# Performance work log

Hardware: AMD Instinct MI355X
Metric: run time of the kernel (lower is better)

The kernel has to match this reference:

```python
import jax, jax.numpy as jnp
import numpy as np

B, D, H = 32768, 512, 512


def setup_inputs() -> dict:
    key = jax.random.key(0)
    ks = jax.random.split(key, 20)
    stdv = 1.0 / np.sqrt(H)

    def u(k, shape):
        return jax.random.uniform(k, shape, jnp.float32, -stdv, stdv)

    inp = {
        "input": jax.random.normal(ks[0], (B, D), jnp.float32),
        "h": jax.random.normal(ks[1], (B, H), jnp.float32),
        "c": jax.random.normal(ks[2], (B, H), jnp.float32),
    }
    names = ["w_ii", "w_hi", "b_ii", "b_hi", "w_if", "w_hf", "b_if", "b_hf",
             "w_ig", "w_hg", "b_ig", "b_hg", "w_io", "w_ho", "b_io", "b_ho"]
    shapes = {"w_i": (D, H), "w_h": (H, H), "b_": (H,)}
    for i, n in enumerate(names):
        shp = (D, H) if n.startswith("w_i") else ((H, H) if n.startswith("w_h") else (H,))
        inp[n] = u(ks[3 + i], shp)
    return inp


def lstm_cell(input, h, c,
              w_ii, w_hi, b_ii, b_hi, w_if, w_hf, b_if, b_hf,
              w_ig, w_hg, b_ig, b_hg, w_io, w_ho, b_io, b_ho):
    # Fuse the 8 small GEMMs into 2 concatenated GEMMs: [B,D]@[D,4H], [B,H]@[H,4H].
    w_x = jnp.concatenate([w_ii, w_if, w_ig, w_io], axis=1)   # [D, 4H]
    w_h = jnp.concatenate([w_hi, w_hf, w_hg, w_ho], axis=1)   # [H, 4H]
    b = jnp.concatenate([b_ii + b_hi, b_if + b_hf, b_ig + b_hg, b_io + b_ho])  # [4H]
    pre = input @ w_x + h @ w_h + b                            # [B, 4H]
    i, f, g, o = jnp.split(pre, 4, axis=1)
    i = jax.nn.sigmoid(i)
    f = jax.nn.sigmoid(f)
    g = jax.nn.sigmoid(g)  # NOTE: source code uses sigmoid here (docstring says tanh)
    o = jax.nn.sigmoid(o)
    c_prime = f * c + i * g
    h_prime = o * jnp.tanh(c_prime)
    return h_prime, c_prime


def reference(input, h, c,
              w_ii, w_hi, b_ii, b_hi, w_if, w_hf, b_if, b_hf,
              w_ig, w_hg, b_ig, b_hg, w_io, w_ho, b_io, b_ho):
    return lstm_cell(input, h, c,
                     w_ii, w_hi, b_ii, b_hi, w_if, w_hf, b_if, b_hf,
                     w_ig, w_hg, b_ig, b_hg, w_io, w_ho, b_io, b_ho)
```

## Files before the change

kernel.cpp:

```cpp
#include <hip/hip_runtime.h>
#include <hip/hip_bf16.h>

typedef __attribute__((ext_vector_type(8))) __bf16 bf16x8;
typedef __attribute__((ext_vector_type(4))) float f32x4;

#define NB 32768
#define HDIM 512
#define KDIM 1024

struct WPtrs { const float* wi[4]; const float* wh[4]; };
struct BPtrs { const float* bi[4]; const float* bh[4]; };

__device__ __forceinline__ float fsigmoid(float x) {
  return 1.0f / (1.0f + __expf(-x));
}
__device__ __forceinline__ float ftanh(float x) {
  return 2.0f / (1.0f + __expf(-2.0f * x)) - 1.0f;
}
__device__ __forceinline__ bf16x8 pack8(float4 a, float4 b) {
  bf16x8 r;
  r[0] = (__bf16)a.x; r[1] = (__bf16)a.y; r[2] = (__bf16)a.z; r[3] = (__bf16)a.w;
  r[4] = (__bf16)b.x; r[5] = (__bf16)b.y; r[6] = (__bf16)b.z; r[7] = (__bf16)b.w;
  return r;
}
__device__ __forceinline__ void gll16(const void* g, void* l) {
  __builtin_amdgcn_global_load_lds(
      (const __attribute__((address_space(1))) void*)g,
      (__attribute__((address_space(3))) void*)l, 16, 0, 0);
}
#define MFMA16(A, B, C) \
  C = __builtin_amdgcn_mfma_f32_16x16x32_bf16(A, B, C, 0, 0, 0)

__global__ void pack_bias_kernel(BPtrs p, float* __restrict__ bias) {
  int idx = blockIdx.x * 256 + threadIdx.x;
  int g = idx >> 9, np = idx & 511;
  bias[idx] = p.bi[g][np] + p.bh[g][np];
}

__global__ void conv_a_kernel(const float* __restrict__ x,
                              const float* __restrict__ h,
                              __bf16* __restrict__ Abf) {
  const size_t N8 = (size_t)NB * KDIM / 8;
  for (size_t i = (size_t)blockIdx.x * blockDim.x + threadIdx.x; i < N8;
       i += (size_t)gridDim.x * blockDim.x) {
    size_t e = i * 8;
    int k = (int)(e & (KDIM - 1));
    size_t r = e >> 10;
    const float* s = (k < 512) ? (x + r * 512 + k) : (h + r * 512 + (k - 512));
    float4 v0 = *(const float4*)s;
    float4 v1 = *(const float4*)(s + 4);
    *(bf16x8*)(Abf + e) = pack8(v0, v1);
  }
}

__global__ void pack_w2_kernel(WPtrs p, __bf16* __restrict__ Wt) {
  __shared__ float tile[64][65];
  const int kt = blockIdx.x;
  const int nt = blockIdx.y;
  const int g = blockIdx.z;
  const int k0 = kt * 64, n0 = nt * 64;
  const float* src = (k0 < 512) ? p.wi[g] : p.wh[g];
  const int k0l = (k0 < 512) ? k0 : (k0 - 512);
  const int rr = threadIdx.x >> 6;
  const int cc = threadIdx.x & 63;
#pragma unroll
  for (int pp = 0; pp < 16; ++pp) {
    int kk = pp * 4 + rr;
    tile[kk][cc] = src[(size_t)(k0l + kk) * 512 + (n0 + cc)];
  }
  __syncthreads();
#pragma unroll
  for (int pp = 0; pp < 16; ++pp) {
    int nn = pp * 4 + rr;
    int np = n0 + nn;
    int prow = (np >> 6) * 256 + ((g >> 1) << 7) + (((np >> 4) & 3) << 5) +
               ((g & 1) << 4) + (np & 15);
    Wt[(size_t)prow * KDIM + (k0 + cc)] = (__bf16)tile[cc][nn];
  }
}

__global__ __launch_bounds__(512, 1) void lstm_gemm2(
    const __bf16* __restrict__ Abf, const __bf16* __restrict__ Wt,
    const float* __restrict__ cin, const float* __restrict__ bias,
    float* __restrict__ out) {
  __shared__ alignas(16) char lds[131072];
  const int tid = threadIdx.x;
  const int wid = tid >> 6;
  const int wm = wid >> 2, wn = wid & 3;
  const int lane = tid & 63;
  const int fc = lane & 15, fg = lane >> 4;

  const int wg = (blockIdx.x & 7) * 128 + (blockIdx.x >> 3);
  const int bm = wg >> 3, bn = wg & 7;

  const __bf16* Asrc = Abf + (size_t)bm * 256 * KDIM;
  const __bf16* Bsrc = Wt + (size_t)bn * 256 * KDIM;

  const int r0 = tid >> 3;
  const int ssl = ((tid & 7) ^ (r0 & 7)) * 8;
  const uint32_t ldst0 = (uint32_t)(tid >> 6) * 1024;

  f32x4 acc[8][4];
#pragma unroll
  for (int m = 0; m < 8; ++m)
#pragma unroll
    for (int n = 0; n < 4; ++n) acc[m][n] = (f32x4){0.f, 0.f, 0.f, 0.f};

  bf16x8 a[4][2], b0[2][2], b1[2][2];

  auto stage = [&](const __bf16* base, int kt, uint32_t lbase) {
    const __bf16* g = base + (size_t)r0 * KDIM + kt * 64 + ssl;
    gll16(g, (void*)&lds[lbase + ldst0]);
    gll16(g + (size_t)64 * KDIM, (void*)&lds[lbase + 8192 + ldst0]);
  };
  auto stA = [&](int kt, int h) {
    if (kt < 16)
      stage(Asrc + (size_t)h * 128 * KDIM, kt,
            (uint32_t)(kt & 1) * 65536 + (uint32_t)h * 16384);
  };
  auto stB = [&](int kt, int h) {
    if (kt < 16)
      stage(Bsrc + (size_t)h * 128 * KDIM, kt,
            (uint32_t)(kt & 1) * 65536 + 32768 + (uint32_t)h * 16384);
  };
  auto ldA = [&](int cb, int h, int mq, int ks) -> bf16x8 {
    int row = wm * 64 + mq * 16 + fc;
    uint32_t off = (uint32_t)cb * 65536 + (uint32_t)h * 16384 +
                   (uint32_t)row * 128 +
                   (uint32_t)(((ks * 4 + fg) ^ (row & 7)) << 4);
    return *(const bf16x8*)&lds[off];
  };
  auto ldB = [&](int cb, int h, int nq, int ks) -> bf16x8 {
    int row = wn * 32 + nq * 16 + fc;
    uint32_t off = (uint32_t)cb * 65536 + 32768 + (uint32_t)h * 16384 +
                   (uint32_t)row * 128 +
                   (uint32_t)(((ks * 4 + fg) ^ (row & 7)) << 4);
    return *(const bf16x8*)&lds[off];
  };

  stA(0, 0); stB(0, 0); stB(0, 1); stA(0, 1);
  stA(1, 0); stB(1, 0); stB(1, 1);
  asm volatile("s_waitcnt vmcnt(6)" ::: "memory");
  __builtin_amdgcn_s_barrier();

#pragma unroll 2
  for (int u = 0; u < 16; ++u) {
    const int cb = u & 1;
#pragma unroll
    for (int mq = 0; mq < 4; ++mq)
#pragma unroll
      for (int ks = 0; ks < 2; ++ks) a[mq][ks] = ldA(cb, 0, mq, ks);
#pragma unroll
    for (int nq = 0; nq < 2; ++nq)
#pragma unroll
      for (int ks = 0; ks < 2; ++ks) b0[nq][ks] = ldB(cb, 0, nq, ks);
    stA(u + 1, 1);
    __builtin_amdgcn_s_barrier();
    asm volatile("s_waitcnt lgkmcnt(0)" ::: "memory");
    __builtin_amdgcn_s_setprio(1);
#pragma unroll
    for (int mq = 0; mq < 4; ++mq)
#pragma unroll
      for (int nq = 0; nq < 2; ++nq)
#pragma unroll
        for (int ks = 0; ks < 2; ++ks)
          MFMA16(a[mq][ks], b0[nq][ks], acc[mq][nq]);
    __builtin_amdgcn_s_setprio(0);
    __builtin_amdgcn_s_barrier();
#pragma unroll
    for (int nq = 0; nq < 2; ++nq)
#pragma unroll
      for (int ks = 0; ks < 2; ++ks) b1[nq][ks] = ldB(cb, 1, nq, ks);
    stA(u + 2, 0);
    __builtin_amdgcn_s_barrier();
    asm volatile("s_waitcnt lgkmcnt(0)" ::: "memory");
    __builtin_amdgcn_s_setprio(1);
#pragma unroll
    for (int mq = 0; mq < 4; ++mq)
#pragma unroll
      for (int nq = 0; nq < 2; ++nq)
#pragma unroll
        for (int ks = 0; ks < 2; ++ks)
          MFMA16(a[mq][ks], b1[nq][ks], acc[mq][2 + nq]);
    __builtin_amdgcn_s_setprio(0);
    __builtin_amdgcn_s_barrier();
#pragma unroll
    for (int mq = 0; mq < 4; ++mq)
#pragma unroll
      for (int ks = 0; ks < 2; ++ks) a[mq][ks] = ldA(cb, 1, mq, ks);
    stB(u + 2, 0);
    __builtin_amdgcn_s_barrier();
    asm volatile("s_waitcnt lgkmcnt(0)" ::: "memory");
    __builtin_amdgcn_s_setprio(1);
#pragma unroll
    for (int mq = 0; mq < 4; ++mq)
#pragma unroll
      for (int nq = 0; nq < 2; ++nq)
#pragma unroll
        for (int ks = 0; ks < 2; ++ks)
          MFMA16(a[mq][ks], b1[nq][ks], acc[4 + mq][2 + nq]);
    __builtin_amdgcn_s_setprio(0);
    __builtin_amdgcn_s_barrier();
    stB(u + 2, 1);
    if (u < 14) {
      asm volatile("s_waitcnt vmcnt(6)" ::: "memory");
    } else if (u == 14) {
      asm volatile("s_waitcnt vmcnt(0)" ::: "memory");
    }
    __builtin_amdgcn_s_barrier();
    __builtin_amdgcn_s_setprio(1);
#pragma unroll
    for (int mq = 0; mq < 4; ++mq)
#pragma unroll
      for (int nq = 0; nq < 2; ++nq)
#pragma unroll
        for (int ks = 0; ks < 2; ++ks)
          MFMA16(a[mq][ks], b0[nq][ks], acc[4 + mq][nq]);
    __builtin_amdgcn_s_setprio(0);
    __builtin_amdgcn_s_barrier();
  }

  const int np = bn * 64 + wn * 16 + fc;
  const float bi = bias[np];
  const float bf_ = bias[512 + np];
  const float bg = bias[1024 + np];
  const float bo = bias[1536 + np];
  const size_t couts = (size_t)NB * HDIM;
#pragma unroll
  for (int mf = 0; mf < 8; ++mf) {
    const int grow0 = bm * 256 + (mf >> 2) * 128 + wm * 64 + (mf & 3) * 16 + fg * 4;
#pragma unroll
    for (int j = 0; j < 4; ++j) {
      const size_t off = (size_t)(grow0 + j) * HDIM + np;
      float i_ = fsigmoid(acc[mf][0][j] + bi);
      float f_ = fsigmoid(acc[mf][1][j] + bf_);
      float g_ = fsigmoid(acc[mf][2][j] + bg);
      float o_ = fsigmoid(acc[mf][3][j] + bo);
      float cp = f_ * cin[off] + i_ * g_;
      out[off] = o_ * ftanh(cp);
      out[couts + off] = cp;
    }
  }
}

__global__ void pack_w1_kernel(WPtrs p, __bf16* __restrict__ Wt) {
  __shared__ float tile[64][65];
  const int kt = blockIdx.x;
  const int nt = blockIdx.y;
  const int g = blockIdx.z;
  const int k0 = kt * 64, n0 = nt * 64;
  const float* src = (k0 < 512) ? p.wi[g] : p.wh[g];
  const int k0l = (k0 < 512) ? k0 : (k0 - 512);
  const int rr = threadIdx.x >> 6;
  const int cc = threadIdx.x & 63;
#pragma unroll
  for (int pp = 0; pp < 16; ++pp) {
    int kk = pp * 4 + rr;
    tile[kk][cc] = src[(size_t)(k0l + kk) * 512 + (n0 + cc)];
  }
  __syncthreads();
#pragma unroll
  for (int pp = 0; pp < 16; ++pp) {
    int nn = pp * 4 + rr;
    int np = n0 + nn;
    int prow = ((np >> 5) << 7) + g * 32 + (np & 31);
    Wt[(size_t)prow * KDIM + (k0 + cc)] = (__bf16)tile[cc][nn];
  }
}

__global__ __launch_bounds__(256) void lstm_gemm1(
    const float* __restrict__ xin, const float* __restrict__ hin,
    const float* __restrict__ cin, const __bf16* __restrict__ Wt,
    const float* __restrict__ bias, float* __restrict__ out) {
  __shared__ alignas(16) __bf16 Alds[2][128 * 32];
  __shared__ alignas(16) __bf16 Blds[2][128 * 32];
  const int tid = threadIdx.x;
  const int w = tid >> 6;
  const int lane = tid & 63;
  const int bid = blockIdx.x;
  const int bm = bid >> 4;
  const int bn = bid & 15;
  f32x4 acc[2][8];
#pragma unroll
  for (int m = 0; m < 2; ++m)
#pragma unroll
    for (int n = 0; n < 8; ++n) acc[m][n] = (f32x4){0.f, 0.f, 0.f, 0.f};
  const int ra = tid >> 2;
  const int q = tid & 3;
  const size_t arow0 = (size_t)(bm * 128 + ra) * 512;
  const size_t arow1 = (size_t)(bm * 128 + ra + 64) * 512;
  const int fc = lane & 15;
  const int fg = lane >> 4;
  const int kg8 = fg * 8;
  {
    const int k = q * 8;
    float4 v0 = *(const float4*)(xin + arow0 + k);
    float4 v1 = *(const float4*)(xin + arow0 + k + 4);
    float4 v2 = *(const float4*)(xin + arow1 + k);
    float4 v3 = *(const float4*)(xin + arow1 + k + 4);
    *(bf16x8*)&Alds[0][ra * 32 + q * 8] = pack8(v0, v1);
    *(bf16x8*)&Alds[0][(ra + 64) * 32 + q * 8] = pack8(v2, v3);
    const __bf16* bs0 = Wt + (size_t)(bn * 128 + ra) * KDIM + q * 8;
    gll16(bs0, (void*)&Blds[0][w * 512]);
    gll16(bs0 + (size_t)64 * KDIM, (void*)&Blds[0][2048 + w * 512]);
  }
  __syncthreads();
#pragma unroll 2
  for (int kt = 0; kt < 32; ++kt) {
    const int cur = kt & 1;
    const int nxt = cur ^ 1;
    float4 v0, v1, v2, v3;
    const bool pf = (kt < 31);
    if (pf) {
      const int kg = (kt + 1) * 32 + q * 8;
      const float* srcb = (kg < 512) ? (xin + kg) : (hin + (kg - 512));
      v0 = *(const float4*)(srcb + arow0);
      v1 = *(const float4*)(srcb + arow0 + 4);
      v2 = *(const float4*)(srcb + arow1);
      v3 = *(const float4*)(srcb + arow1 + 4);
      const __bf16* bs0 =
          Wt + (size_t)(bn * 128 + ra) * KDIM + (kt + 1) * 32 + q * 8;
      gll16(bs0, (void*)&Blds[nxt][w * 512]);
      gll16(bs0 + (size_t)64 * KDIM, (void*)&Blds[nxt][2048 + w * 512]);
    }
    bf16x8 af0 = *(const bf16x8*)&Alds[cur][(w * 32 + fc) * 32 + kg8];
    bf16x8 af1 = *(const bf16x8*)&Alds[cur][(w * 32 + 16 + fc) * 32 + kg8];
#pragma unroll
    for (int nf = 0; nf < 8; ++nf) {
      bf16x8 bfrag = *(const bf16x8*)&Blds[cur][(nf * 16 + fc) * 32 + kg8];
      MFMA16(af0, bfrag, acc[0][nf]);
      MFMA16(af1, bfrag, acc[1][nf]);
    }
    if (pf) {
      *(bf16x8*)&Alds[nxt][ra * 32 + q * 8] = pack8(v0, v1);
      *(bf16x8*)&Alds[nxt][(ra + 64) * 32 + q * 8] = pack8(v2, v3);
    }
    __syncthreads();
  }
  const size_t couts = (size_t)NB * HDIM;
#pragma unroll
  for (int nn = 0; nn < 2; ++nn) {
    const int np = bn * 32 + nn * 16 + fc;
    const float bi = bias[np];
    const float bff = bias[512 + np];
    const float bg = bias[1024 + np];
    const float bo = bias[1536 + np];
#pragma unroll
    for (int m = 0; m < 2; ++m) {
      const int rbase = bm * 128 + w * 32 + m * 16 + fg * 4;
#pragma unroll
      for (int j = 0; j < 4; ++j) {
        const size_t off = (size_t)(rbase + j) * HDIM + np;
        float i_ = fsigmoid(acc[m][nn][j] + bi);
        float f_ = fsigmoid(acc[m][2 + nn][j] + bff);
        float g_ = fsigmoid(acc[m][4 + nn][j] + bg);
        float o_ = fsigmoid(acc[m][6 + nn][j] + bo);
        float cp = f_ * cin[off] + i_ * g_;
        float hp = o_ * ftanh(cp);
        out[off] = hp;
        out[couts + off] = cp;
      }
    }
  }
}

extern "C" void kernel_launch(void* const* d_in, const int* in_sizes, int n_in,
                              void* d_out, int out_size, void* d_ws,
                              size_t ws_size, hipStream_t stream) {
  const float* xin = (const float*)d_in[0];
  const float* hin = (const float*)d_in[1];
  const float* cin = (const float*)d_in[2];
  WPtrs wp;
  wp.wi[0] = (const float*)d_in[3];
  wp.wi[1] = (const float*)d_in[7];
  wp.wi[2] = (const float*)d_in[11];
  wp.wi[3] = (const float*)d_in[15];
  wp.wh[0] = (const float*)d_in[4];
  wp.wh[1] = (const float*)d_in[8];
  wp.wh[2] = (const float*)d_in[12];
  wp.wh[3] = (const float*)d_in[16];
  BPtrs bp;
  bp.bi[0] = (const float*)d_in[5];
  bp.bi[1] = (const float*)d_in[9];
  bp.bi[2] = (const float*)d_in[13];
  bp.bi[3] = (const float*)d_in[17];
  bp.bh[0] = (const float*)d_in[6];
  bp.bh[1] = (const float*)d_in[10];
  bp.bh[2] = (const float*)d_in[14];
  bp.bh[3] = (const float*)d_in[18];

  const size_t needA = (size_t)NB * KDIM * 2;
  const size_t needW = (size_t)2048 * KDIM * 2;
  const size_t needBias = (size_t)4 * HDIM * 4;

  if (ws_size >= needA + needW + needBias) {
    __bf16* Abf = (__bf16*)d_ws;
    __bf16* Wt = (__bf16*)((char*)d_ws + needA);
    float* bias = (float*)((char*)d_ws + needA + needW);
    conv_a_kernel<<<2048, 256, 0, stream>>>(xin, hin, Abf);
    pack_w2_kernel<<<dim3(16, 8, 4), 256, 0, stream>>>(wp, Wt);
    pack_bias_kernel<<<8, 256, 0, stream>>>(bp, bias);
    lstm_gemm2<<<1024, 512, 0, stream>>>(Abf, Wt, cin, bias, (float*)d_out);
  } else {
    __bf16* Wt = (__bf16*)d_ws;
    float* bias = (float*)((char*)d_ws + needW);
    pack_w1_kernel<<<dim3(16, 8, 4), 256, 0, stream>>>(wp, Wt);
    pack_bias_kernel<<<8, 256, 0, stream>>>(bp, bias);
    lstm_gemm1<<<4096, 256, 0, stream>>>(xin, hin, cin, Wt, bias,
                                         (float*)d_out);
  }
}
```

Before: 214.2 us.

## Make GEMM persistent over four M-tiles per block with continuous pipeline

The main GEMM now launches 256 blocks instead of 1024. Each block walks four consecutive 256-row M tiles for its N column, running one continuous 64-step K pipeline that prefetches across tile boundaries. After each tile it runs the LSTM epilogue and resets the accumulators. This removes per-block pipeline fill and drain and launch tail effects, at the cost of fewer blocks (256, about one per CU), and the epilogue now stalls the pipeline mid-loop. The small-workspace fallback path and the gemm1 and pack_w1 kernels are deleted, so the code now assumes the workspace is large enough.

```diff
diff --git a/kernel.cpp b/kernel.cpp
--- a/kernel.cpp
+++ b/kernel.cpp
@@ -79,7 +79,7 @@
   }
 }
 
-__global__ __launch_bounds__(512, 1) void lstm_gemm2(
+__global__ __launch_bounds__(512, 1) void lstm_gemm3(
     const __bf16* __restrict__ Abf, const __bf16* __restrict__ Wt,
     const float* __restrict__ cin, const float* __restrict__ bias,
     float* __restrict__ out) {
@@ -90,10 +90,9 @@
   const int lane = tid & 63;
   const int fc = lane & 15, fg = lane >> 4;
 
-  const int wg = (blockIdx.x & 7) * 128 + (blockIdx.x >> 3);
-  const int bm = wg >> 3, bn = wg & 7;
-
-  const __bf16* Asrc = Abf + (size_t)bm * 256 * KDIM;
+  const int bn = blockIdx.x & 7;
+  const int bmg = blockIdx.x >> 3;
+
   const __bf16* Bsrc = Wt + (size_t)bn * 256 * KDIM;
 
   const int r0 = tid >> 3;
@@ -108,20 +107,26 @@
 
   bf16x8 a[4][2], b0[2][2], b1[2][2];
 
-  auto stage = [&](const __bf16* base, int kt, uint32_t lbase) {
-    const __bf16* g = base + (size_t)r0 * KDIM + kt * 64 + ssl;
-    gll16(g, (void*)&lds[lbase + ldst0]);
-    gll16(g + (size_t)64 * KDIM, (void*)&lds[lbase + 8192 + ldst0]);
-  };
-  auto stA = [&](int kt, int h) {
-    if (kt < 16)
-      stage(Asrc + (size_t)h * 128 * KDIM, kt,
-            (uint32_t)(kt & 1) * 65536 + (uint32_t)h * 16384);
-  };
-  auto stB = [&](int kt, int h) {
-    if (kt < 16)
-      stage(Bsrc + (size_t)h * 128 * KDIM, kt,
-            (uint32_t)(kt & 1) * 65536 + 32768 + (uint32_t)h * 16384);
+  auto stA = [&](int t, int h) {
+    if (t < 64) {
+      const __bf16* g = Abf +
+                        ((size_t)((bmg << 2) + (t >> 4)) * 256 + h * 128 + r0) *
+                            KDIM +
+                        (t & 15) * 64 + ssl;
+      uint32_t lb = (uint32_t)(t & 1) * 65536 + (uint32_t)h * 16384 + ldst0;
+      gll16(g, (void*)&lds[lb]);
+      gll16(g + (size_t)64 * KDIM, (void*)&lds[lb + 8192]);
+    }
+  };
+  auto stB = [&](int t, int h) {
+    if (t < 64) {
+      const __bf16* g =
+          Bsrc + ((size_t)h * 128 + r0) * KDIM + (t & 15) * 64 + ssl;
+      uint32_t lb =
+          (uint32_t)(t & 1) * 65536 + 32768 + (uint32_t)h * 16384 + ldst0;
+      gll16(g, (void*)&lds[lb]);
+      gll16(g + (size_t)64 * KDIM, (void*)&lds[lb + 8192]);
+    }
   };
   auto ldA = [&](int cb, int h, int mq, int ks) -> bf16x8 {
     int row = wm * 64 + mq * 16 + fc;
@@ -138,227 +143,113 @@
     return *(const bf16x8*)&lds[off];
   };
 
-  stA(0, 0); stB(0, 0); stB(0, 1); stA(0, 1);
-  stA(1, 0); stB(1, 0); stB(1, 1);
-  asm volatile("s_waitcnt vmcnt(6)" ::: "memory");
-  __builtin_amdgcn_s_barrier();
-
-#pragma unroll 2
-  for (int u = 0; u < 16; ++u) {
-    const int cb = u & 1;
-#pragma unroll
-    for (int mq = 0; mq < 4; ++mq)
-#pragma unroll
-      for (int ks = 0; ks < 2; ++ks) a[mq][ks] = ldA(cb, 0, mq, ks);
-#pragma unroll
-    for (int nq = 0; nq < 2; ++nq)
-#pragma unroll
-      for (int ks = 0; ks < 2; ++ks) b0[nq][ks] = ldB(cb, 0, nq, ks);
-    stA(u + 1, 1);
-    __builtin_amdgcn_s_barrier();
-    asm volatile("s_waitcnt lgkmcnt(0)" ::: "memory");
-    __builtin_amdgcn_s_setprio(1);
-#pragma unroll
-    for (int mq = 0; mq < 4; ++mq)
-#pragma unroll
-      for (int nq = 0; nq < 2; ++nq)
-#pragma unroll
-        for (int ks = 0; ks < 2; ++ks)
-          MFMA16(a[mq][ks], b0[nq][ks], acc[mq][nq]);
-    __builtin_amdgcn_s_setprio(0);
-    __builtin_amdgcn_s_barrier();
-#pragma unroll
-    for (int nq = 0; nq < 2; ++nq)
-#pragma unroll
-      for (int ks = 0; ks < 2; ++ks) b1[nq][ks] = ldB(cb, 1, nq, ks);
-    stA(u + 2, 0);
-    __builtin_amdgcn_s_barrier();
-    asm volatile("s_waitcnt lgkmcnt(0)" ::: "memory");
-    __builtin_amdgcn_s_setprio(1);
-#pragma unroll
-    for (int mq = 0; mq < 4; ++mq)
-#pragma unroll
-      for (int nq = 0; nq < 2; ++nq)
-#pragma unroll
-        for (int ks = 0; ks < 2; ++ks)
-          MFMA16(a[mq][ks], b1[nq][ks], acc[mq][2 + nq]);
-    __builtin_amdgcn_s_setprio(0);
-    __builtin_amdgcn_s_barrier();
-#pragma unroll
-    for (int mq = 0; mq < 4; ++mq)
-#pragma unroll
-      for (int ks = 0; ks < 2; ++ks) a[mq][ks] = ldA(cb, 1, mq, ks);
-    stB(u + 2, 0);
-    __builtin_amdgcn_s_barrier();
-    asm volatile("s_waitcnt lgkmcnt(0)" ::: "memory");
-    __builtin_amdgcn_s_setprio(1);
-#pragma unroll
-    for (int mq = 0; mq < 4; ++mq)
-#pragma unroll
-      for (int nq = 0; nq < 2; ++nq)
-#pragma unroll
-        for (int ks = 0; ks < 2; ++ks)
-          MFMA16(a[mq][ks], b1[nq][ks], acc[4 + mq][2 + nq]);
-    __builtin_amdgcn_s_setprio(0);
-    __builtin_amdgcn_s_barrier();
-    stB(u + 2, 1);
-    if (u < 14) {
-      asm volatile("s_waitcnt vmcnt(6)" ::: "memory");
-    } else if (u == 14) {
-      asm volatile("s_waitcnt vmcnt(0)" ::: "memory");
-    }
-    __builtin_amdgcn_s_barrier();
-    __builtin_amdgcn_s_setprio(1);
-#pragma unroll
-    for (int mq = 0; mq < 4; ++mq)
-#pragma unroll
-      for (int nq = 0; nq < 2; ++nq)
-#pragma unroll
-        for (int ks = 0; ks < 2; ++ks)
-          MFMA16(a[mq][ks], b0[nq][ks], acc[4 + mq][nq]);
-    __builtin_amdgcn_s_setprio(0);
-    __builtin_amdgcn_s_barrier();
-  }
-
   const int np = bn * 64 + wn * 16 + fc;
   const float bi = bias[np];
   const float bf_ = bias[512 + np];
   const float bg = bias[1024 + np];
   const float bo = bias[1536 + np];
   const size_t couts = (size_t)NB * HDIM;
-#pragma unroll
-  for (int mf = 0; mf < 8; ++mf) {
-    const int grow0 = bm * 256 + (mf >> 2) * 128 + wm * 64 + (mf & 3) * 16 + fg * 4;
-#pragma unroll
-    for (int j = 0; j < 4; ++j) {
-      const size_t off = (size_t)(grow0 + j) * HDIM + np;
-      float i_ = fsigmoid(acc[mf][0][j] + bi);
-      float f_ = fsigmoid(acc[mf][1][j] + bf_);
-      float g_ = fsigmoid(acc[mf][2][j] + bg);
-      float o_ = fsigmoid(acc[mf][3][j] + bo);
-      float cp = f_ * cin[off] + i_ * g_;
-      out[off] = o_ * ftanh(cp);
-      out[couts + off] = cp;
-    }
-  }
-}
-
-__global__ void pack_w1_kernel(WPtrs p, __bf16* __restrict__ Wt) {
-  __shared__ float tile[64][65];
-  const int kt = blockIdx.x;
-  const int nt = blockIdx.y;
-  const int g = blockIdx.z;
-  const int k0 = kt * 64, n0 = nt * 64;
-  const float* src = (k0 < 512) ? p.wi[g] : p.wh[g];
-  const int k0l = (k0 < 512) ? k0 : (k0 - 512);
-  const int rr = threadIdx.x >> 6;
-  const int cc = threadIdx.x & 63;
-#pragma unroll
-  for (int pp = 0; pp < 16; ++pp) {
-    int kk = pp * 4 + rr;
-    tile[kk][cc] = src[(size_t)(k0l + kk) * 512 + (n0 + cc)];
-  }
-  __syncthreads();
-#pragma unroll
-  for (int pp = 0; pp < 16; ++pp) {
-    int nn = pp * 4 + rr;
-    int np = n0 + nn;
-    int prow = ((np >> 5) << 7) + g * 32 + (np & 31);
-    Wt[(size_t)prow * KDIM + (k0 + cc)] = (__bf16)tile[cc][nn];
-  }
-}
-
-__global__ __launch_bounds__(256) void lstm_gemm1(
-    const float* __restrict__ xin, const float* __restrict__ hin,
-    const float* __restrict__ cin, const __bf16* __restrict__ Wt,
-    const float* __restrict__ bias, float* __restrict__ out) {
-  __shared__ alignas(16) __bf16 Alds[2][128 * 32];
-  __shared__ alignas(16) __bf16 Blds[2][128 * 32];
-  const int tid = threadIdx.x;
-  const int w = tid >> 6;
-  const int lane = tid & 63;
-  const int bid = blockIdx.x;
-  const int bm = bid >> 4;
-  const int bn = bid & 15;
-  f32x4 acc[2][8];
-#pragma unroll
-  for (int m = 0; m < 2; ++m)
-#pragma unroll
-    for (int n = 0; n < 8; ++n) acc[m][n] = (f32x4){0.f, 0.f, 0.f, 0.f};
-  const int ra = tid >> 2;
-  const int q = tid & 3;
-  const size_t arow0 = (size_t)(bm * 128 + ra) * 512;
-  const size_t arow1 = (size_t)(bm * 128 + ra + 64) * 512;
-  const int fc = lane & 15;
-  const int fg = lane >> 4;
-  const int kg8 = fg * 8;
-  {
-    const int k = q * 8;
-    float4 v0 = *(const float4*)(xin + arow0 + k);
-    float4 v1 = *(const float4*)(xin + arow0 + k + 4);
-    float4 v2 = *(const float4*)(xin + arow1 + k);
-    float4 v3 = *(const float4*)(xin + arow1 + k + 4);
-    *(bf16x8*)&Alds[0][ra * 32 + q * 8] = pack8(v0, v1);
-    *(bf16x8*)&Alds[0][(ra + 64) * 32 + q * 8] = pack8(v2, v3);
-    const __bf16* bs0 = Wt + (size_t)(bn * 128 + ra) * KDIM + q * 8;
-    gll16(bs0, (void*)&Blds[0][w * 512]);
-    gll16(bs0 + (size_t)64 * KDIM, (void*)&Blds[0][2048 + w * 512]);
-  }
-  __syncthreads();
+
+  stA(0, 0); stB(0, 0); stB(0, 1); stA(0, 1);
+  stA(1, 0); stB(1, 0); stB(1, 1);
+  asm volatile("s_waitcnt vmcnt(6)" ::: "memory");
+  __builtin_amdgcn_s_barrier();
+
 #pragma unroll 2
-  for (int kt = 0; kt < 32; ++kt) {
-    const int cur = kt & 1;
-    const int nxt = cur ^ 1;
-    float4 v0, v1, v2, v3;
-    const bool pf = (kt < 31);
-    if (pf) {
-      const int kg = (kt + 1) * 32 + q * 8;
-      const float* srcb = (kg < 512) ? (xin + kg) : (hin + (kg - 512));
-      v0 = *(const float4*)(srcb + arow0);
-      v1 = *(const float4*)(srcb + arow0 + 4);
-      v2 = *(const float4*)(srcb + arow1);
-      v3 = *(const float4*)(srcb + arow1 + 4);
-      const __bf16* bs0 =
-          Wt + (size_t)(bn * 128 + ra) * KDIM + (kt + 1) * 32 + q * 8;
-      gll16(bs0, (void*)&Blds[nxt][w * 512]);
-      gll16(bs0 + (size_t)64 * KDIM, (void*)&Blds[nxt][2048 + w * 512]);
-    }
-    bf16x8 af0 = *(const bf16x8*)&Alds[cur][(w * 32 + fc) * 32 + kg8];
-    bf16x8 af1 = *(const bf16x8*)&Alds[cur][(w * 32 + 16 + fc) * 32 + kg8];
-#pragma unroll
-    for (int nf = 0; nf < 8; ++nf) {
-      bf16x8 bfrag = *(const bf16x8*)&Blds[cur][(nf * 16 + fc) * 32 + kg8];
-      MFMA16(af0, bfrag, acc[0][nf]);
-      MFMA16(af1, bfrag, acc[1][nf]);
-    }
-    if (pf) {
-      *(bf16x8*)&Alds[nxt][ra * 32 + q * 8] = pack8(v0, v1);
-      *(bf16x8*)&Alds[nxt][(ra + 64) * 32 + q * 8] = pack8(v2, v3);
-    }
-    __syncthreads();
-  }
-  const size_t couts = (size_t)NB * HDIM;
-#pragma unroll
-  for (int nn = 0; nn < 2; ++nn) {
-    const int np = bn * 32 + nn * 16 + fc;
-    const float bi = bias[np];
-    const float bff = bias[512 + np];
-    const float bg = bias[1024 + np];
-    const float bo = bias[1536 + np];
-#pragma unroll
-    for (int m = 0; m < 2; ++m) {
-      const int rbase = bm * 128 + w * 32 + m * 16 + fg * 4;
-#pragma unroll
-      for (int j = 0; j < 4; ++j) {
-        const size_t off = (size_t)(rbase + j) * HDIM + np;
-        float i_ = fsigmoid(acc[m][nn][j] + bi);
-        float f_ = fsigmoid(acc[m][2 + nn][j] + bff);
-        float g_ = fsigmoid(acc[m][4 + nn][j] + bg);
-        float o_ = fsigmoid(acc[m][6 + nn][j] + bo);
-        float cp = f_ * cin[off] + i_ * g_;
-        float hp = o_ * ftanh(cp);
-        out[off] = hp;
-        out[couts + off] = cp;
+  for (int t = 0; t < 64; ++t) {
+    const int cb = t & 1;
+#pragma unroll
+    for (int mq = 0; mq < 4; ++mq)
+#pragma unroll
+      for (int ks = 0; ks < 2; ++ks) a[mq][ks] = ldA(cb, 0, mq, ks);
+#pragma unroll
+    for (int nq = 0; nq < 2; ++nq)
+#pragma unroll
+      for (int ks = 0; ks < 2; ++ks) b0[nq][ks] = ldB(cb, 0, nq, ks);
+    stA(t + 1, 1);
+    __builtin_amdgcn_s_barrier();
+    asm volatile("s_waitcnt lgkmcnt(0)" ::: "memory");
+    __builtin_amdgcn_s_setprio(1);
+#pragma unroll
+    for (int mq = 0; mq < 4; ++mq)
+#pragma unroll
+      for (int nq = 0; nq < 2; ++nq)
+#pragma unroll
+        for (int ks = 0; ks < 2; ++ks)
+          MFMA16(a[mq][ks], b0[nq][ks], acc[mq][nq]);
+    __builtin_amdgcn_s_setprio(0);
+    __builtin_amdgcn_s_barrier();
+#pragma unroll
+    for (int nq = 0; nq < 2; ++nq)
+#pragma unroll
+      for (int ks = 0; ks < 2; ++ks) b1[nq][ks] = ldB(cb, 1, nq, ks);
+    stA(t + 2, 0);
+    __builtin_amdgcn_s_barrier();
+    asm volatile("s_waitcnt lgkmcnt(0)" ::: "memory");
+    __builtin_amdgcn_s_setprio(1);
+#pragma unroll
+    for (int mq = 0; mq < 4; ++mq)
+#pragma unroll
+      for (int nq = 0; nq < 2; ++nq)
+#pragma unroll
+        for (int ks = 0; ks < 2; ++ks)
+          MFMA16(a[mq][ks], b1[nq][ks], acc[mq][2 + nq]);
+    __builtin_amdgcn_s_setprio(0);
+    __builtin_amdgcn_s_barrier();
+#pragma unroll
+    for (int mq = 0; mq < 4; ++mq)
+#pragma unroll
+      for (int ks = 0; ks < 2; ++ks) a[mq][ks] = ldA(cb, 1, mq, ks);
+    stB(t + 2, 0);
+    __builtin_amdgcn_s_barrier();
+    asm volatile("s_waitcnt lgkmcnt(0)" ::: "memory");
+    __builtin_amdgcn_s_setprio(1);
+#pragma unroll
+    for (int mq = 0; mq < 4; ++mq)
+#pragma unroll
+      for (int nq = 0; nq < 2; ++nq)
+#pragma unroll
+        for (int ks = 0; ks < 2; ++ks)
+          MFMA16(a[mq][ks], b1[nq][ks], acc[4 + mq][2 + nq]);
+    __builtin_amdgcn_s_setprio(0);
+    __builtin_amdgcn_s_barrier();
+    stB(t + 2, 1);
+    if (t < 62) {
+      asm volatile("s_waitcnt vmcnt(6)" ::: "memory");
+    } else if (t == 62) {
+      asm volatile("s_waitcnt vmcnt(0)" ::: "memory");
+    }
+    __builtin_amdgcn_s_barrier();
+    __builtin_amdgcn_s_setprio(1);
+#pragma unroll
+    for (int mq = 0; mq < 4; ++mq)
+#pragma unroll
+      for (int nq = 0; nq < 2; ++nq)
+#pragma unroll
+        for (int ks = 0; ks < 2; ++ks)
+          MFMA16(a[mq][ks], b0[nq][ks], acc[4 + mq][nq]);
+    __builtin_amdgcn_s_setprio(0);
+    __builtin_amdgcn_s_barrier();
+
+    if ((t & 15) == 15) {
+      const int g = t >> 4;
+#pragma unroll
+      for (int mf = 0; mf < 8; ++mf) {
+        const int grow0 = ((bmg << 2) + g) * 256 + (mf >> 2) * 128 + wm * 64 +
+                          (mf & 3) * 16 + fg * 4;
+#pragma unroll
+        for (int j = 0; j < 4; ++j) {
+          const size_t off = (size_t)(grow0 + j) * HDIM + np;
+          float i_ = fsigmoid(acc[mf][0][j] + bi);
+          float f_ = fsigmoid(acc[mf][1][j] + bf_);
+          float g_ = fsigmoid(acc[mf][2][j] + bg);
+          float o_ = fsigmoid(acc[mf][3][j] + bo);
+          float cp = f_ * cin[off] + i_ * g_;
+          out[off] = o_ * ftanh(cp);
+          out[couts + off] = cp;
+        }
+#pragma unroll
+        for (int n = 0; n < 4; ++n) acc[mf][n] = (f32x4){0.f, 0.f, 0.f, 0.f};
       }
     }
   }
@@ -391,22 +282,13 @@
 
   const size_t needA = (size_t)NB * KDIM * 2;
   const size_t needW = (size_t)2048 * KDIM * 2;
-  const size_t needBias = (size_t)4 * HDIM * 4;
-
-  if (ws_size >= needA + needW + needBias) {
-    __bf16* Abf = (__bf16*)d_ws;
-    __bf16* Wt = (__bf16*)((char*)d_ws + needA);
-    float* bias = (float*)((char*)d_ws + needA + needW);
-    conv_a_kernel<<<2048, 256, 0, stream>>>(xin, hin, Abf);
-    pack_w2_kernel<<<dim3(16, 8, 4), 256, 0, stream>>>(wp, Wt);
-    pack_bias_kernel<<<8, 256, 0, stream>>>(bp, bias);
-    lstm_gemm2<<<1024, 512, 0, stream>>>(Abf, Wt, cin, bias, (float*)d_out);
-  } else {
-    __bf16* Wt = (__bf16*)d_ws;
-    float* bias = (float*)((char*)d_ws + needW);
-    pack_w1_kernel<<<dim3(16, 8, 4), 256, 0, stream>>>(wp, Wt);
-    pack_bias_kernel<<<8, 256, 0, stream>>>(bp, bias);
-    lstm_gemm1<<<4096, 256, 0, stream>>>(xin, hin, cin, Wt, bias,
-                                         (float*)d_out);
-  }
-}
+
+  __bf16* Abf = (__bf16*)d_ws;
+  __bf16* Wt = (__bf16*)((char*)d_ws + needA);
+  float* bias = (float*)((char*)d_ws + needA + needW);
+
+  conv_a_kernel<<<2048, 256, 0, stream>>>(xin, hin, Abf);
+  pack_w2_kernel<<<dim3(16, 8, 4), 256, 0, stream>>>(wp, Wt);
+  pack_bias_kernel<<<8, 256, 0, stream>>>(bp, bias);
+  lstm_gemm3<<<256, 512, 0, stream>>>(Abf, Wt, cin, bias, (float*)d_out);
+}
```

New measurement: 213.8 us. Within noise of the previous version (-0.2%).
